# Performance work log

Measured on AMD Instinct MI355X. Metric: run time of the kernel, lower is better.

Reference implementation:

```python
import jax, jax.numpy as jnp
import numpy as np

N = 50000      # nodes
E = 800000     # edges
D = 128        # in_dim == out_dim
H = 8          # heads
DH = D // H    # head dim = 16
BN_EPS = 1e-5


def batch_norm(x, gamma, beta):
    # BatchNorm1d in training mode: biased variance over the node/batch axis.
    mu = jnp.mean(x, axis=0)
    var = jnp.mean((x - mu) ** 2, axis=0)
    return (x - mu) * jax.lax.rsqrt(var + BN_EPS) * gamma + beta


def setup_inputs() -> dict:
    key = jax.random.key(0)
    ks = jax.random.split(key, 16)
    inp = {
        'src': jax.random.randint(ks[0], (E,), 0, N),
        'dst': jax.random.randint(ks[1], (E,), 0, N),
        'h': jax.random.normal(ks[2], (N, D), jnp.float32),
        'e': jax.random.normal(ks[3], (E, D), jnp.float32),
        'h_in': jax.random.normal(ks[4], (N, D), jnp.float32),  # unused: overwritten by h in forward
        # attention projections (bias=False)
        'Wq': jax.random.normal(ks[5], (D, D), jnp.float32) / np.sqrt(D),
        'Wk': jax.random.normal(ks[6], (D, D), jnp.float32) / np.sqrt(D),
        'Wv': jax.random.normal(ks[7], (D, D), jnp.float32) / np.sqrt(D),
        'We': jax.random.normal(ks[8], (D, D), jnp.float32) / np.sqrt(D),
        # sdp_layer (bias=True)
        'W_sdp': jax.random.normal(ks[9], (D, D), jnp.float32) / np.sqrt(D),
        'b_sdp': jnp.zeros((D,), jnp.float32),
        # FFN out_h / out_h_2
        'W_h1': jax.random.normal(ks[10], (D, 2 * D), jnp.float32) / np.sqrt(D),
        'b_h1': jnp.zeros((2 * D,), jnp.float32),
        'W_h2': jax.random.normal(ks[11], (2 * D, D), jnp.float32) / np.sqrt(2 * D),
        'b_h2': jnp.zeros((D,), jnp.float32),
        # batch_norm_1 (shared across both BN applications)
        'bn_gamma': jnp.ones((D,), jnp.float32),
        'bn_beta': jnp.zeros((D,), jnp.float32),
    }
    return inp


def reference(src, dst, h, e, h_in, Wq, Wk, Wv, We, W_sdp, b_sdp,
              W_h1, b_h1, W_h2, b_h2, bn_gamma, bn_beta):
    h_res = h  # h_in = h inside forward

    # --- MultiHeadAttention (default path: all edges real, sum aggregation) ---
    q = (h @ Wq).reshape(N, H, DH)
    k = (h @ Wk).reshape(N, H, DH)
    v = (h @ Wv).reshape(N, H, DH)   # v = v_linear(h_in) with h_in == h
    ef = (e @ We).reshape(E, H, DH)

    # src_dot_dst -> scaling -> imp_exp_attn: elementwise K_src*Q_dst / sqrt(dh) * E
    score = (k[src] * q[dst]) / np.sqrt(DH) * ef          # [E, H, DH]
    # exp('score'): exp(clamp(sum_d score, -5, 5)), keepdim
    score_soft = jnp.exp(jnp.clip(score.sum(-1), -5.0, 5.0))[..., None]  # [E, H, 1]

    aV = jax.ops.segment_sum(v[src] * score_soft, dst, num_segments=N)   # [N, H, DH]
    z = jax.ops.segment_sum(score_soft, dst, num_segments=N)             # [N, H, 1]
    h_attn = (aV / (z + 1e-6)).reshape(N, D)

    # --- EncoderLayer post-attention (dropout=0 -> identity) ---
    hx = h_attn @ W_sdp + b_sdp
    hx = h_res + hx
    hx = batch_norm(hx, bn_gamma, bn_beta)

    h_in2 = hx
    ff = jax.nn.relu(hx @ W_h1 + b_h1) @ W_h2 + b_h2
    hx = h_in2 + ff
    hx = batch_norm(hx, bn_gamma, bn_beta)

    # edge_learning=False: e returned unchanged
    return hx, e
```

## Files before the change

### kernel.cpp

```cpp
#include <hip/hip_runtime.h>
#include <hip/hip_bf16.h>
#include <math.h>

#define N_NODES 50000
#define E_EDGES 800000
#define D_DIM   128
#define H_HEADS 8

typedef __attribute__((ext_vector_type(8))) short short8;
typedef __attribute__((ext_vector_type(4))) float f32x4;
typedef unsigned int   uint_t;
typedef unsigned short ushort_t;

static __device__ __forceinline__ float4 ldg4(const float* p) {
    return *reinterpret_cast<const float4*>(p);
}
static __device__ __forceinline__ ushort_t f2bf(float x) {
    union { float f; uint_t u; } v; v.f = x;
    uint_t r = v.u + 0x7fffu + ((v.u >> 16) & 1u);
    return (ushort_t)(r >> 16);
}
static __device__ __forceinline__ float bf2f(ushort_t b) {
    union { uint_t u; float f; } v; v.u = ((uint_t)b) << 16;
    return v.f;
}
static __device__ __forceinline__ uint_t pk(float lo, float hi) {
    return (uint_t)f2bf(lo) | ((uint_t)f2bf(hi) << 16);
}

__global__ void hist_kernel(const int* __restrict__ dst, int* __restrict__ hist) {
    int i = blockIdx.x * blockDim.x + threadIdx.x;
    if (i < E_EDGES) atomicAdd(&hist[dst[i]], 1);
}

__global__ __launch_bounds__(1024) void scan_kernel(const int* __restrict__ cnt,
                                                    int* __restrict__ start,
                                                    int* __restrict__ cursor) {
    __shared__ int sh[1024];
    const int t = threadIdx.x;
    const int CPT = (N_NODES + 1023) / 1024;
    int lo = t * CPT;
    int hi = lo + CPT; if (hi > N_NODES) hi = N_NODES; if (lo > N_NODES) lo = N_NODES;
    int s = 0;
    for (int i = lo; i < hi; i++) s += cnt[i];
    sh[t] = s;
    __syncthreads();
    for (int off = 1; off < 1024; off <<= 1) {
        int v = (t >= off) ? sh[t - off] : 0;
        __syncthreads();
        sh[t] += v;
        __syncthreads();
    }
    int run = sh[t] - s;
    for (int i = lo; i < hi; i++) {
        start[i]  = run;
        cursor[i] = run;
        run += cnt[i];
    }
    if (t == 1023) start[N_NODES] = sh[1023];
}

__global__ void scatter_kernel(const int* __restrict__ src, const int* __restrict__ dst,
                               int* __restrict__ cursor,
                               int* __restrict__ rank, int* __restrict__ srcs) {
    int i = blockIdx.x * blockDim.x + threadIdx.x;
    if (i < E_EDGES) {
        int p = atomicAdd(&cursor[dst[i]], 1);
        rank[i] = p;
        srcs[p] = src[i];
    }
}

__global__ __launch_bounds__(256) void prep_weights(const float* __restrict__ Wq,
                                                    const float* __restrict__ Wk,
                                                    const float* __restrict__ Wv,
                                                    const float* __restrict__ We,
                                                    const float* __restrict__ Wsdp,
                                                    const float* __restrict__ Wh1,
                                                    const float* __restrict__ Wh2,
                                                    ushort_t* __restrict__ prep) {
    const int b = blockIdx.x;
    const float* W; int ld, cb, kc;
    if (b < 6)       { W = (b < 2 ? Wq : (b < 4 ? Wk : Wv)); ld = 128; cb = 0; kc = b & 1; }
    else if (b < 8)  { W = We;   ld = 128; cb = 0;            kc = b - 6; }
    else if (b < 10) { W = Wsdp; ld = 128; cb = 0;            kc = b - 8; }
    else if (b < 14) { W = Wh1;  ld = 256; cb = (b - 10) >> 1; kc = (b - 10) & 1; }
    else             { W = Wh2;  ld = 128; cb = 0;            kc = b - 14; }
    char* tile = (char*)(prep + (size_t)b * 8192);
    for (int i = threadIdx.x; i < 8192; i += 256) {
        int col = i >> 6, kl = i & 63;
        int k = kc * 64 + kl;
        float v = W[(size_t)k * ld + cb * 128 + col];
        int byte = (col * 128 + kl * 2) ^ ((col & 7) << 4);
        *(ushort_t*)(tile + byte) = f2bf(v);
    }
}

__global__ __launch_bounds__(256) void prep_we_frag(const float* __restrict__ We,
                                                    ushort_t* __restrict__ WeF) {
    int slot = blockIdx.x * 256 + threadIdx.x;
    if (slot < 2048) {
        int lane = slot & 63;
        int kc   = (slot >> 6) & 3;
        int cg   = slot >> 8;
        int col  = cg * 16 + (lane & 15);
        int kb   = kc * 32 + ((lane >> 4) << 3);
#pragma unroll
        for (int j = 0; j < 8; j++)
            WeF[slot * 8 + j] = f2bf(We[(size_t)(kb + j) * 128 + col]);
    }
}

template<int ROWS, int OBF, int ABF, int RESMODE, int SADD, int ASS>
__global__ __launch_bounds__(256) void gemm_bf16(const void* __restrict__ Av,
                                                 int M, int K,
                                                 const ushort_t* __restrict__ Bt, int nkc,
                                                 const float* __restrict__ bias,
                                                 const void* __restrict__ residv,
                                                 void* __restrict__ Cv, int ldc,
                                                 size_t cbStride, int doRelu,
                                                 float* __restrict__ sums,
                                                 const float* __restrict__ ss) {
    constexpr int MI  = ROWS / 32;
    constexpr int TPR = 256 / ROWS;
    constexpr int KPT = 64 / TPR;
    __shared__ __align__(16) unsigned char As[ROWS * 128];
    __shared__ __align__(16) unsigned char Bs[16384];
    __shared__ float csum[128], csq[128];
    const int tid  = threadIdx.x;
    const int lane = tid & 63;
    const int wid  = tid >> 6;
    const int wr   = wid >> 1;
    const int wc   = wid & 1;
    const int cb   = blockIdx.y;
    const int row0 = blockIdx.x * ROWS;

    if (SADD && tid < 128) { csum[tid] = 0.f; csq[tid] = 0.f; }

    f32x4 acc[MI][4];
#pragma unroll
    for (int i = 0; i < MI; i++)
#pragma unroll
        for (int j = 0; j < 4; j++) acc[i][j] = (f32x4){0.f, 0.f, 0.f, 0.f};

    for (int kc = 0; kc < nkc; kc++) {
        __syncthreads();
        {
            int row = tid / TPR;
            int kl0 = (tid % TPR) * KPT;
            int gr  = row0 + row;
            int s = (row & 7) << 4;
            if (ABF) {
                const ushort_t* A16 = (const ushort_t*)Av;
#pragma unroll
                for (int j = 0; j < KPT / 8; j++) {
                    uint4 w = make_uint4(0, 0, 0, 0);
                    if (gr < M) w = *(const uint4*)(&A16[(size_t)gr * K + kc * 64 + kl0 + 8 * j]);
                    int byte = (row * 128 + (kl0 + 8 * j) * 2) ^ s;
                    *(uint4*)(As + byte) = w;
                }
            } else {
                const float* A = (const float*)Av;
                float4 v4[KPT / 4];
                if (gr < M) {
                    const float* ap = &A[(size_t)gr * K + kc * 64 + kl0];
#pragma unroll
                    for (int j = 0; j < KPT / 4; j++) v4[j] = ldg4(ap + 4 * j);
                } else {
#pragma unroll
                    for (int j = 0; j < KPT / 4; j++) v4[j] = make_float4(0.f, 0.f, 0.f, 0.f);
                }
                if (ASS) {
#pragma unroll
                    for (int j = 0; j < KPT / 4; j++) {
                        int kk = kc * 64 + kl0 + 4 * j;
                        v4[j].x = v4[j].x * ss[kk + 0] + ss[128 + kk + 0];
                        v4[j].y = v4[j].y * ss[kk + 1] + ss[128 + kk + 1];
                        v4[j].z = v4[j].z * ss[kk + 2] + ss[128 + kk + 2];
                        v4[j].w = v4[j].w * ss[kk + 3] + ss[128 + kk + 3];
                    }
                }
#pragma unroll
                for (int j = 0; j < KPT / 8; j++) {
                    uint4 w;
                    w.x = pk(v4[2 * j].x, v4[2 * j].y);
                    w.y = pk(v4[2 * j].z, v4[2 * j].w);
                    w.z = pk(v4[2 * j + 1].x, v4[2 * j + 1].y);
                    w.w = pk(v4[2 * j + 1].z, v4[2 * j + 1].w);
                    int byte = (row * 128 + (kl0 + 8 * j) * 2) ^ s;
                    *(uint4*)(As + byte) = w;
                }
            }
        }
        {
            const uint4* gB = (const uint4*)(Bt + (size_t)(cb * nkc + kc) * 8192);
#pragma unroll
            for (int j = 0; j < 4; j++) {
                int idx = j * 256 + tid;
                ((uint4*)Bs)[idx] = gB[idx];
            }
        }
        __syncthreads();
#pragma unroll
        for (int k0 = 0; k0 < 64; k0 += 32) {
            short8 a[MI], b[4];
#pragma unroll
            for (int mi = 0; mi < MI; mi++) {
                int row = wr * (ROWS / 2) + mi * 16 + (lane & 15);
                int byte = (row * 128 + k0 * 2 + (lane >> 4) * 16) ^ ((row & 7) << 4);
                a[mi] = *(const short8*)(As + byte);
            }
#pragma unroll
            for (int ni = 0; ni < 4; ni++) {
                int col = wc * 64 + ni * 16 + (lane & 15);
                int byte = (col * 128 + k0 * 2 + (lane >> 4) * 16) ^ ((col & 7) << 4);
                b[ni] = *(const short8*)(Bs + byte);
            }
#pragma unroll
            for (int mi = 0; mi < MI; mi++)
#pragma unroll
                for (int ni = 0; ni < 4; ni++)
                    acc[mi][ni] = __builtin_amdgcn_mfma_f32_16x16x32_bf16(a[mi], b[ni], acc[mi][ni], 0, 0, 0);
        }
    }

    float colS[4] = {0.f, 0.f, 0.f, 0.f};
    float colQ[4] = {0.f, 0.f, 0.f, 0.f};
#pragma unroll
    for (int mi = 0; mi < MI; mi++) {
#pragma unroll
        for (int r = 0; r < 4; r++) {
            int row = row0 + wr * (ROWS / 2) + mi * 16 + ((lane >> 4) << 2) + r;
            if (row < M) {
#pragma unroll
                for (int ni = 0; ni < 4; ni++) {
                    int col = wc * 64 + ni * 16 + (lane & 15);
                    float v = acc[mi][ni][r];
                    if (bias) v += bias[cb * 128 + col];
                    if (doRelu) v = fmaxf(v, 0.f);
                    if (residv) {
                        if (RESMODE == 1) {
                            v += bf2f(((const ushort_t*)residv)[(size_t)row * ldc + col]);
                        } else if (RESMODE == 2) {
                            float rr = ((const float*)residv)[(size_t)row * ldc + col];
                            v += rr * ss[col] + ss[128 + col];
                        } else {
                            v += ((const float*)residv)[(size_t)row * ldc + col];
                        }
                    }
                    if (SADD) { colS[ni] += v; colQ[ni] += v * v; }
                    if (OBF) ((ushort_t*)Cv)[cb * cbStride + (size_t)row * ldc + col] = f2bf(v);
                    else     ((float*)Cv)[cb * cbStride + (size_t)row * ldc + col] = v;
                }
            }
        }
    }
    if (SADD) {
#pragma unroll
        for (int ni = 0; ni < 4; ni++) {
            int col = wc * 64 + ni * 16 + (lane & 15);
            atomicAdd(&csum[col], colS[ni]);
            atomicAdd(&csq[col],  colQ[ni]);
        }
        __syncthreads();
        if (tid < 128) {
            atomicAdd(&sums[tid],       csum[tid]);
            atomicAdd(&sums[128 + tid], csq[tid]);
        }
    }
}

__global__ __launch_bounds__(256, 7) void edge_mfma(const float* __restrict__ e,
                                                    const int* __restrict__ src,
                                                    const int* __restrict__ dst,
                                                    const ushort_t* __restrict__ Qm,
                                                    const ushort_t* __restrict__ Km,
                                                    const ushort_t* __restrict__ WeF,
                                                    const int* __restrict__ rank,
                                                    float* __restrict__ S,
                                                    float* __restrict__ out_e) {
    __shared__ __align__(16) unsigned char Asm[16384];
    __shared__ float sm[64][8];
    const int tid  = threadIdx.x;
    const int lane = tid & 63;
    const int wid  = tid >> 6;
    const int wr   = wid >> 1;
    const int wc   = wid & 1;
    const int e0   = blockIdx.x * 64;

    {
        int row = tid >> 2;
        int c0  = (tid & 3) * 32;
        const float* ep = &e[(size_t)(e0 + row) * 128 + c0];
        float*       op = &out_e[(size_t)(e0 + row) * 128 + c0];
        float4 v4[8];
#pragma unroll
        for (int j = 0; j < 8; j++) v4[j] = ldg4(ep + 4 * j);
#pragma unroll
        for (int j = 0; j < 8; j++) *(float4*)(op + 4 * j) = v4[j];
        int s = (row & 7) << 4;
#pragma unroll
        for (int g = 0; g < 2; g++) {
            int cc    = c0 + 16 * g;
            int chunk = cc >> 6;
            int klb   = (cc & 63) * 2;
            uint4 w0, w1;
            w0.x = pk(v4[4 * g + 0].x, v4[4 * g + 0].y); w0.y = pk(v4[4 * g + 0].z, v4[4 * g + 0].w);
            w0.z = pk(v4[4 * g + 1].x, v4[4 * g + 1].y); w0.w = pk(v4[4 * g + 1].z, v4[4 * g + 1].w);
            w1.x = pk(v4[4 * g + 2].x, v4[4 * g + 2].y); w1.y = pk(v4[4 * g + 2].z, v4[4 * g + 2].w);
            w1.z = pk(v4[4 * g + 3].x, v4[4 * g + 3].y); w1.w = pk(v4[4 * g + 3].z, v4[4 * g + 3].w);
            *(uint4*)(Asm + chunk * 8192 + ((row * 128 + klb) ^ s))      = w0;
            *(uint4*)(Asm + chunk * 8192 + ((row * 128 + klb + 16) ^ s)) = w1;
        }
    }
    __syncthreads();

    f32x4 acc[2][4];
#pragma unroll
    for (int i = 0; i < 2; i++)
#pragma unroll
        for (int j = 0; j < 4; j++) acc[i][j] = (f32x4){0.f, 0.f, 0.f, 0.f};

#pragma unroll
    for (int k0 = 0; k0 < 128; k0 += 32) {
        int chunk = k0 >> 6;
        int klb   = (k0 & 63) * 2;
        int kc    = k0 >> 5;
        short8 a[2];
#pragma unroll
        for (int mi = 0; mi < 2; mi++) {
            int arow = wr * 32 + mi * 16 + (lane & 15);
            int byte = chunk * 8192 + ((arow * 128 + klb + (lane >> 4) * 16) ^ ((arow & 7) << 4));
            a[mi] = *(const short8*)(Asm + byte);
        }
#pragma unroll
        for (int ni = 0; ni < 4; ni++) {
            int cg = wc * 4 + ni;
            short8 b = *(const short8*)(WeF + ((size_t)((cg * 4 + kc) * 64 + lane)) * 8);
#pragma unroll
            for (int mi = 0; mi < 2; mi++)
                acc[mi][ni] = __builtin_amdgcn_mfma_f32_16x16x32_bf16(a[mi], b, acc[mi][ni], 0, 0, 0);
        }
    }

#pragma unroll
    for (int mi = 0; mi < 2; mi++) {
        int rows[4], sidx[4], didx[4];
#pragma unroll
        for (int r = 0; r < 4; r++) {
            rows[r] = e0 + wr * 32 + mi * 16 + ((lane >> 4) << 2) + r;
            sidx[r] = src[rows[r]];
            didx[r] = dst[rows[r]];
        }
#pragma unroll
        for (int ni = 0; ni < 4; ni++) {
            int head = wc * 4 + ni;
            int col  = head * 16 + (lane & 15);
            float pv[4];
#pragma unroll
            for (int r = 0; r < 4; r++) {
                float kv = bf2f(Km[(size_t)sidx[r] * 128 + col]);
                float qv = bf2f(Qm[(size_t)didx[r] * 128 + col]);
                pv[r] = acc[mi][ni][r] * kv * qv;
            }
#pragma unroll
            for (int off = 1; off < 16; off <<= 1)
#pragma unroll
                for (int r = 0; r < 4; r++) pv[r] += __shfl_xor(pv[r], off, 64);
            if ((lane & 15) == 0) {
#pragma unroll
                for (int r = 0; r < 4; r++) {
                    float v = fminf(fmaxf(0.25f * pv[r], -5.f), 5.f);
                    sm[rows[r] - e0][head] = __expf(v);
                }
            }
        }
    }
    __syncthreads();
    if (tid < 64) {
        int rk = rank[e0 + tid];
        float4 a0 = *(const float4*)&sm[tid][0];
        float4 a1 = *(const float4*)&sm[tid][4];
        *(float4*)&S[(size_t)rk * 8]     = a0;
        *(float4*)&S[(size_t)rk * 8 + 4] = a1;
    }
}

__global__ __launch_bounds__(256) void agg_kernel(const uint_t* __restrict__ Vu,
                                                  const float* __restrict__ S,
                                                  const int* __restrict__ start,
                                                  const int* __restrict__ srcs,
                                                  uint_t* __restrict__ HAu) {
    const int lane = threadIdx.x & 63;
    const int n = blockIdx.x * 4 + (threadIdx.x >> 6);
    if (n >= N_NODES) return;
    const int s0 = start[n];
    const int s1 = start[n + 1];
    const int h  = lane >> 3;
    float a0 = 0.f, a1 = 0.f, z = 0.f;
    int i = s0;
    for (; i + 4 <= s1; i += 4) {
        int m0 = srcs[i], m1 = srcs[i + 1], m2 = srcs[i + 2], m3 = srcs[i + 3];
        float t0 = S[(size_t)i * 8 + h];
        float t1 = S[(size_t)(i + 1) * 8 + h];
        float t2 = S[(size_t)(i + 2) * 8 + h];
        float t3 = S[(size_t)(i + 3) * 8 + h];
        uint_t v0 = Vu[(size_t)m0 * 64 + lane];
        uint_t v1 = Vu[(size_t)m1 * 64 + lane];
        uint_t v2 = Vu[(size_t)m2 * 64 + lane];
        uint_t v3 = Vu[(size_t)m3 * 64 + lane];
        a0 = fmaf(t0, bf2f((ushort_t)v0), a0); a1 = fmaf(t0, bf2f((ushort_t)(v0 >> 16)), a1);
        a0 = fmaf(t1, bf2f((ushort_t)v1), a0); a1 = fmaf(t1, bf2f((ushort_t)(v1 >> 16)), a1);
        a0 = fmaf(t2, bf2f((ushort_t)v2), a0); a1 = fmaf(t2, bf2f((ushort_t)(v2 >> 16)), a1);
        a0 = fmaf(t3, bf2f((ushort_t)v3), a0); a1 = fmaf(t3, bf2f((ushort_t)(v3 >> 16)), a1);
        z += t0 + t1 + t2 + t3;
    }
    for (; i < s1; i++) {
        int m = srcs[i];
        float t = S[(size_t)i * 8 + h];
        uint_t v = Vu[(size_t)m * 64 + lane];
        a0 = fmaf(t, bf2f((ushort_t)v), a0);
        a1 = fmaf(t, bf2f((ushort_t)(v >> 16)), a1);
        z += t;
    }
    float inv = 1.f / (z + 1e-6f);
    HAu[(size_t)n * 64 + lane] = pk(a0 * inv, a1 * inv);
}

__global__ void bn_finalize(const float* __restrict__ sums,
                            const float* __restrict__ gamma,
                            const float* __restrict__ beta,
                            float* __restrict__ ss) {
    int c = threadIdx.x;
    float mu  = sums[c] * (1.f / (float)N_NODES);
    float var = sums[128 + c] * (1.f / (float)N_NODES) - mu * mu;
    float scale = rsqrtf(var + 1e-5f) * gamma[c];
    ss[c]       = scale;
    ss[128 + c] = beta[c] - mu * scale;
}

__global__ __launch_bounds__(256) void bn_apply_f32(const float* __restrict__ X,
                                                    const float* __restrict__ ss,
                                                    float* __restrict__ Y) {
    const size_t total = (size_t)N_NODES * 128;
    const size_t step = (size_t)gridDim.x * blockDim.x * 4;
    for (size_t i = ((size_t)blockIdx.x * blockDim.x + threadIdx.x) * 4; i < total; i += step) {
        float4 x = ldg4(&X[i]);
        int c = (int)(i & 127);
        float4 y;
        y.x = x.x * ss[c + 0] + ss[128 + c + 0];
        y.y = x.y * ss[c + 1] + ss[128 + c + 1];
        y.z = x.z * ss[c + 2] + ss[128 + c + 2];
        y.w = x.w * ss[c + 3] + ss[128 + c + 3];
        *(float4*)(&Y[i]) = y;
    }
}

extern "C" void kernel_launch(void* const* d_in, const int* in_sizes, int n_in,
                              void* d_out, int out_size, void* d_ws, size_t ws_size,
                              hipStream_t stream) {
    (void)in_sizes; (void)n_in; (void)out_size; (void)ws_size;
    const int*   src   = (const int*)d_in[0];
    const int*   dst   = (const int*)d_in[1];
    const float* h     = (const float*)d_in[2];
    const float* e     = (const float*)d_in[3];
    const float* Wq    = (const float*)d_in[5];
    const float* Wk    = (const float*)d_in[6];
    const float* Wv    = (const float*)d_in[7];
    const float* We    = (const float*)d_in[8];
    const float* Wsdp  = (const float*)d_in[9];
    const float* bsdp  = (const float*)d_in[10];
    const float* Wh1   = (const float*)d_in[11];
    const float* bh1   = (const float*)d_in[12];
    const float* Wh2   = (const float*)d_in[13];
    const float* bh2   = (const float*)d_in[14];
    const float* gamma = (const float*)d_in[15];
    const float* beta  = (const float*)d_in[16];
    float* out = (float*)d_out;

    float* ws = (float*)d_ws;
    const size_t NM = (size_t)N_NODES * 128;
    ushort_t* Q16  = (ushort_t*)ws;
    ushort_t* K16  = Q16 + NM;
    ushort_t* V16  = Q16 + 2 * NM;
    ushort_t* HA16 = (ushort_t*)(ws + 3 * NM / 2);
    float*    Kb   = ws + 2 * NM;
    float*    Sb   = ws + 3 * NM;
    float*    T1r  = ws + 4 * NM;
    ushort_t* T16  = (ushort_t*)T1r;
    float*    STATS = ws + 6 * NM;
    int* hist   = (int*)(STATS + 1024);
    int* startp = hist + N_NODES;
    int* cursor = startp + N_NODES + 1;
    ushort_t* prep = (ushort_t*)(((uintptr_t)(cursor + N_NODES) + 255) & ~(uintptr_t)255);
    ushort_t* WeF  = prep + (size_t)18 * 8192;

    int* rank = (int*)T1r;
    int* srcs = rank + E_EDGES;

    float* sums1 = STATS;
    float* ss1   = STATS + 256;
    float* sums2 = STATS + 512;
    float* ss2   = STATS + 768;

    prep_weights<<<18, 256, 0, stream>>>(Wq, Wk, Wv, We, Wsdp, Wh1, Wh2, prep);
    prep_we_frag<<<8, 256, 0, stream>>>(We, WeF);

    hipMemsetAsync(STATS, 0, (1024 + N_NODES) * sizeof(float), stream);

    hist_kernel<<<(E_EDGES + 255) / 256, 256, 0, stream>>>(dst, hist);
    scan_kernel<<<1, 1024, 0, stream>>>(hist, startp, cursor);
    scatter_kernel<<<(E_EDGES + 255) / 256, 256, 0, stream>>>(src, dst, cursor, rank, srcs);

    const int rt128 = (N_NODES + 127) / 128;
    const int rt64  = (N_NODES + 63) / 64;

    gemm_bf16<128, 1, 0, 0, 0, 0><<<dim3(rt128, 3), 256, 0, stream>>>(
        h, N_NODES, 128, prep, 2, nullptr, nullptr, Q16, 128, NM, 0, nullptr, nullptr);

    edge_mfma<<<E_EDGES / 64, 256, 0, stream>>>(e, src, dst, Q16, K16, WeF,
                                                rank, Sb, out + NM);

    agg_kernel<<<(N_NODES + 3) / 4, 256, 0, stream>>>((const uint_t*)V16, Sb, startp, srcs,
                                                      (uint_t*)HA16);

    gemm_bf16<64, 0, 1, 0, 1, 0><<<dim3(rt64, 1), 256, 0, stream>>>(
        HA16, N_NODES, 128, prep + (size_t)8 * 8192, 2, bsdp, h, Kb, 128, 0, 0, sums1, nullptr);

    bn_finalize<<<1, 128, 0, stream>>>(sums1, gamma, beta, ss1);

    gemm_bf16<128, 1, 0, 0, 0, 1><<<dim3(rt128, 2), 256, 0, stream>>>(
        Kb, N_NODES, 128, prep + (size_t)10 * 8192, 2, bh1, nullptr, T16, 256, 128, 1, nullptr, ss1);
    gemm_bf16<64, 0, 1, 2, 1, 0><<<dim3(rt64, 1), 256, 0, stream>>>(
        T16, N_NODES, 256, prep + (size_t)14 * 8192, 4, bh2, Kb, Kb, 128, 0, 0, sums2, ss1);

    bn_finalize<<<1, 128, 0, stream>>>(sums2, gamma, beta, ss2);
    bn_apply_f32<<<2048, 256, 0, stream>>>(Kb, ss2, out);
}
```

Baseline: 837.6 us.

## Store edge attention scores as bf16 and remap edge warps to full rows

```diff
diff --git a/kernel.cpp b/kernel.cpp
--- a/kernel.cpp
+++ b/kernel.cpp
@@ -270,124 +270,104 @@
     }
 }
 
-__global__ __launch_bounds__(256, 7) void edge_mfma(const float* __restrict__ e,
+__global__ __launch_bounds__(256, 6) void edge_mfma(const float* __restrict__ e,
                                                     const int* __restrict__ src,
                                                     const int* __restrict__ dst,
                                                     const ushort_t* __restrict__ Qm,
                                                     const ushort_t* __restrict__ Km,
                                                     const ushort_t* __restrict__ WeF,
                                                     const int* __restrict__ rank,
-                                                    float* __restrict__ S,
+                                                    ushort_t* __restrict__ S16,
                                                     float* __restrict__ out_e) {
     __shared__ __align__(16) unsigned char Asm[16384];
-    __shared__ float sm[64][8];
     const int tid  = threadIdx.x;
     const int lane = tid & 63;
     const int wid  = tid >> 6;
-    const int wr   = wid >> 1;
-    const int wc   = wid & 1;
     const int e0   = blockIdx.x * 64;
 
-    {
-        int row = tid >> 2;
-        int c0  = (tid & 3) * 32;
+#pragma unroll
+    for (int it = 0; it < 2; it++) {
+        int row = (tid >> 3) + it * 32;
+        int c0  = (tid & 7) * 16;
         const float* ep = &e[(size_t)(e0 + row) * 128 + c0];
         float*       op = &out_e[(size_t)(e0 + row) * 128 + c0];
-        float4 v4[8];
-#pragma unroll
-        for (int j = 0; j < 8; j++) v4[j] = ldg4(ep + 4 * j);
-#pragma unroll
-        for (int j = 0; j < 8; j++) *(float4*)(op + 4 * j) = v4[j];
-        int s = (row & 7) << 4;
-#pragma unroll
-        for (int g = 0; g < 2; g++) {
-            int cc    = c0 + 16 * g;
-            int chunk = cc >> 6;
-            int klb   = (cc & 63) * 2;
-            uint4 w0, w1;
-            w0.x = pk(v4[4 * g + 0].x, v4[4 * g + 0].y); w0.y = pk(v4[4 * g + 0].z, v4[4 * g + 0].w);
-            w0.z = pk(v4[4 * g + 1].x, v4[4 * g + 1].y); w0.w = pk(v4[4 * g + 1].z, v4[4 * g + 1].w);
-            w1.x = pk(v4[4 * g + 2].x, v4[4 * g + 2].y); w1.y = pk(v4[4 * g + 2].z, v4[4 * g + 2].w);
-            w1.z = pk(v4[4 * g + 3].x, v4[4 * g + 3].y); w1.w = pk(v4[4 * g + 3].z, v4[4 * g + 3].w);
-            *(uint4*)(Asm + chunk * 8192 + ((row * 128 + klb) ^ s))      = w0;
-            *(uint4*)(Asm + chunk * 8192 + ((row * 128 + klb + 16) ^ s)) = w1;
-        }
+        float4 v4[4];
+#pragma unroll
+        for (int j = 0; j < 4; j++) v4[j] = ldg4(ep + 4 * j);
+#pragma unroll
+        for (int j = 0; j < 4; j++) *(float4*)(op + 4 * j) = v4[j];
+        int chunk = c0 >> 6;
+        int klb   = (c0 & 63) * 2;
+        int s     = (row & 7) << 4;
+        uint4 w0, w1;
+        w0.x = pk(v4[0].x, v4[0].y); w0.y = pk(v4[0].z, v4[0].w);
+        w0.z = pk(v4[1].x, v4[1].y); w0.w = pk(v4[1].z, v4[1].w);
+        w1.x = pk(v4[2].x, v4[2].y); w1.y = pk(v4[2].z, v4[2].w);
+        w1.z = pk(v4[3].x, v4[3].y); w1.w = pk(v4[3].z, v4[3].w);
+        *(uint4*)(Asm + chunk * 8192 + ((row * 128 + klb) ^ s))      = w0;
+        *(uint4*)(Asm + chunk * 8192 + ((row * 128 + klb + 16) ^ s)) = w1;
     }
     __syncthreads();
 
-    f32x4 acc[2][4];
-#pragma unroll
-    for (int i = 0; i < 2; i++)
-#pragma unroll
-        for (int j = 0; j < 4; j++) acc[i][j] = (f32x4){0.f, 0.f, 0.f, 0.f};
+    f32x4 acc[8];
+#pragma unroll
+    for (int i = 0; i < 8; i++) acc[i] = (f32x4){0.f, 0.f, 0.f, 0.f};
 
 #pragma unroll
     for (int k0 = 0; k0 < 128; k0 += 32) {
         int chunk = k0 >> 6;
         int klb   = (k0 & 63) * 2;
         int kc    = k0 >> 5;
-        short8 a[2];
-#pragma unroll
-        for (int mi = 0; mi < 2; mi++) {
-            int arow = wr * 32 + mi * 16 + (lane & 15);
+        short8 a;
+        {
+            int arow = wid * 16 + (lane & 15);
             int byte = chunk * 8192 + ((arow * 128 + klb + (lane >> 4) * 16) ^ ((arow & 7) << 4));
-            a[mi] = *(const short8*)(Asm + byte);
-        }
-#pragma unroll
-        for (int ni = 0; ni < 4; ni++) {
-            int cg = wc * 4 + ni;
-            short8 b = *(const short8*)(WeF + ((size_t)((cg * 4 + kc) * 64 + lane)) * 8);
-#pragma unroll
-            for (int mi = 0; mi < 2; mi++)
-                acc[mi][ni] = __builtin_amdgcn_mfma_f32_16x16x32_bf16(a[mi], b, acc[mi][ni], 0, 0, 0);
-        }
-    }
-
-#pragma unroll
-    for (int mi = 0; mi < 2; mi++) {
-        int rows[4], sidx[4], didx[4];
+            a = *(const short8*)(Asm + byte);
+        }
+#pragma unroll
+        for (int ni = 0; ni < 8; ni++) {
+            short8 b = *(const short8*)(WeF + ((size_t)((ni * 4 + kc) * 64 + lane)) * 8);
+            acc[ni] = __builtin_amdgcn_mfma_f32_16x16x32_bf16(a, b, acc[ni], 0, 0, 0);
+        }
+    }
+
+    const int rows0 = e0 + wid * 16 + ((lane >> 4) << 2);
+    int sidx[4], didx[4];
+#pragma unroll
+    for (int r = 0; r < 4; r++) {
+        sidx[r] = src[rows0 + r];
+        didx[r] = dst[rows0 + r];
+    }
+    const int myr = lane & 15;
+    float sc[8];
+#pragma unroll
+    for (int ni = 0; ni < 8; ni++) {
+        int col = ni * 16 + (lane & 15);
+        float pv[4];
 #pragma unroll
         for (int r = 0; r < 4; r++) {
-            rows[r] = e0 + wr * 32 + mi * 16 + ((lane >> 4) << 2) + r;
-            sidx[r] = src[rows[r]];
-            didx[r] = dst[rows[r]];
-        }
-#pragma unroll
-        for (int ni = 0; ni < 4; ni++) {
-            int head = wc * 4 + ni;
-            int col  = head * 16 + (lane & 15);
-            float pv[4];
-#pragma unroll
-            for (int r = 0; r < 4; r++) {
-                float kv = bf2f(Km[(size_t)sidx[r] * 128 + col]);
-                float qv = bf2f(Qm[(size_t)didx[r] * 128 + col]);
-                pv[r] = acc[mi][ni][r] * kv * qv;
-            }
-#pragma unroll
-            for (int off = 1; off < 16; off <<= 1)
-#pragma unroll
-                for (int r = 0; r < 4; r++) pv[r] += __shfl_xor(pv[r], off, 64);
-            if ((lane & 15) == 0) {
-#pragma unroll
-                for (int r = 0; r < 4; r++) {
-                    float v = fminf(fmaxf(0.25f * pv[r], -5.f), 5.f);
-                    sm[rows[r] - e0][head] = __expf(v);
-                }
-            }
-        }
-    }
-    __syncthreads();
-    if (tid < 64) {
-        int rk = rank[e0 + tid];
-        float4 a0 = *(const float4*)&sm[tid][0];
-        float4 a1 = *(const float4*)&sm[tid][4];
-        *(float4*)&S[(size_t)rk * 8]     = a0;
-        *(float4*)&S[(size_t)rk * 8 + 4] = a1;
+            float kv = bf2f(Km[(size_t)sidx[r] * 128 + col]);
+            float qv = bf2f(Qm[(size_t)didx[r] * 128 + col]);
+            pv[r] = acc[ni][r] * kv * qv;
+        }
+#pragma unroll
+        for (int off = 1; off < 16; off <<= 1)
+#pragma unroll
+            for (int r = 0; r < 4; r++) pv[r] += __shfl_xor(pv[r], off, 64);
+        float mv = (myr == 0) ? pv[0] : (myr == 1) ? pv[1] : (myr == 2) ? pv[2] : pv[3];
+        sc[ni] = __expf(fminf(fmaxf(0.25f * mv, -5.f), 5.f));
+    }
+    if (myr < 4) {
+        int rk = rank[rows0 + myr];
+        uint4 u;
+        u.x = pk(sc[0], sc[1]); u.y = pk(sc[2], sc[3]);
+        u.z = pk(sc[4], sc[5]); u.w = pk(sc[6], sc[7]);
+        *(uint4*)&S16[(size_t)rk * 8] = u;
     }
 }
 
 __global__ __launch_bounds__(256) void agg_kernel(const uint_t* __restrict__ Vu,
-                                                  const float* __restrict__ S,
+                                                  const ushort_t* __restrict__ S16,
                                                   const int* __restrict__ start,
                                                   const int* __restrict__ srcs,
                                                   uint_t* __restrict__ HAu) {
@@ -401,10 +381,10 @@
     int i = s0;
     for (; i + 4 <= s1; i += 4) {
         int m0 = srcs[i], m1 = srcs[i + 1], m2 = srcs[i + 2], m3 = srcs[i + 3];
-        float t0 = S[(size_t)i * 8 + h];
-        float t1 = S[(size_t)(i + 1) * 8 + h];
-        float t2 = S[(size_t)(i + 2) * 8 + h];
-        float t3 = S[(size_t)(i + 3) * 8 + h];
+        float t0 = bf2f(S16[(size_t)i * 8 + h]);
+        float t1 = bf2f(S16[(size_t)(i + 1) * 8 + h]);
+        float t2 = bf2f(S16[(size_t)(i + 2) * 8 + h]);
+        float t3 = bf2f(S16[(size_t)(i + 3) * 8 + h]);
         uint_t v0 = Vu[(size_t)m0 * 64 + lane];
         uint_t v1 = Vu[(size_t)m1 * 64 + lane];
         uint_t v2 = Vu[(size_t)m2 * 64 + lane];
@@ -417,7 +397,7 @@
     }
     for (; i < s1; i++) {
         int m = srcs[i];
-        float t = S[(size_t)i * 8 + h];
+        float t = bf2f(S16[(size_t)i * 8 + h]);
         uint_t v = Vu[(size_t)m * 64 + lane];
         a0 = fmaf(t, bf2f((ushort_t)v), a0);
         a1 = fmaf(t, bf2f((ushort_t)(v >> 16)), a1);
@@ -485,7 +465,7 @@
     ushort_t* V16  = Q16 + 2 * NM;
     ushort_t* HA16 = (ushort_t*)(ws + 3 * NM / 2);
     float*    Kb   = ws + 2 * NM;
-    float*    Sb   = ws + 3 * NM;
+    ushort_t* S16  = (ushort_t*)(ws + 3 * NM);
     float*    T1r  = ws + 4 * NM;
     ushort_t* T16  = (ushort_t*)T1r;
     float*    STATS = ws + 6 * NM;
@@ -519,9 +499,9 @@
         h, N_NODES, 128, prep, 2, nullptr, nullptr, Q16, 128, NM, 0, nullptr, nullptr);
 
     edge_mfma<<<E_EDGES / 64, 256, 0, stream>>>(e, src, dst, Q16, K16, WeF,
-                                                rank, Sb, out + NM);
-
-    agg_kernel<<<(N_NODES + 3) / 4, 256, 0, stream>>>((const uint_t*)V16, Sb, startp, srcs,
+                                                rank, S16, out + NM);
+
+    agg_kernel<<<(N_NODES + 3) / 4, 256, 0, stream>>>((const uint_t*)V16, S16, startp, srcs,
                                                       (uint_t*)HA16);
 
     gemm_bf16<64, 0, 1, 0, 1, 0><<<dim3(rt64, 1), 256, 0, stream>>>(
```

New measurement: 787.3 us. 1.06x faster.
